# Kernel tuning notes

Hardware: AMD Instinct MI355X
Metric: run time of the kernel (lower is better)

The kernel has to match this reference:

```python
import jax, jax.numpy as jnp
import numpy as np

N_NODES = 100000
N_PART = 5000
N_EDGES = 1000000
D_NODE = 128
D_PART = 128
D_ATT = 20


def setup_inputs() -> dict:
    key = jax.random.key(0)
    ks = jax.random.split(key, 20)
    inp = {
        "nodes_hidden": jax.random.normal(ks[0], (N_NODES, D_NODE), jnp.float32),
        "particles_hidden": jax.random.normal(ks[1], (N_PART, D_PART), jnp.float32),
        "global_rep": jax.random.normal(ks[2], (N_PART, D_NODE), jnp.float32),
        "src": jax.random.randint(ks[3], (N_EDGES,), 0, N_NODES, jnp.int32),
        "dst": jax.random.randint(ks[4], (N_EDGES,), 0, N_PART, jnp.int32),
        "key_W": jax.random.normal(ks[5], (D_NODE, D_ATT), jnp.float32) * 0.05,
        "key_b": jnp.zeros((D_ATT,), jnp.float32),
        "val_W": jax.random.normal(ks[6], (D_NODE, D_PART), jnp.float32) * 0.05,
        "val_b": jnp.zeros((D_PART,), jnp.float32),
        "q_W": jax.random.normal(ks[7], (D_PART + D_NODE, D_ATT), jnp.float32) * 0.05,
        "q_b": jnp.zeros((D_ATT,), jnp.float32),
        "W_ih": jax.random.normal(ks[8], (3 * D_PART, D_PART), jnp.float32) * 0.05,
        "W_hh": jax.random.normal(ks[9], (3 * D_PART, D_PART), jnp.float32) * 0.05,
        "b_ih": jnp.zeros((3 * D_PART,), jnp.float32),
        "b_hh": jnp.zeros((3 * D_PART,), jnp.float32),
        "ln_g": jnp.ones((D_PART,), jnp.float32),
        "ln_b": jnp.zeros((D_PART,), jnp.float32),
        "mlp_W1": jax.random.normal(ks[10], (D_PART, 64), jnp.float32) * 0.05,
        "mlp_b1": jnp.zeros((64,), jnp.float32),
        "mlp_W2": jax.random.normal(ks[11], (64, D_PART), jnp.float32) * 0.05,
        "mlp_b2": jnp.zeros((D_PART,), jnp.float32),
    }
    return inp


def reference(nodes_hidden, particles_hidden, global_rep, src, dst,
              key_W, key_b, val_W, val_b, q_W, q_b,
              W_ih, W_hh, b_ih, b_hh, ln_g, ln_b,
              mlp_W1, mlp_b1, mlp_W2, mlp_b2):
    norm = jnp.float32(1.0) / jnp.sqrt(jnp.float32(D_ATT))
    keys = nodes_hidden @ key_W + key_b          # [N, 20]
    vals = nodes_hidden @ val_W + val_b          # [N, P]
    q_in = jnp.concatenate([particles_hidden, global_rep], axis=1)
    query = q_in @ q_W + q_b                     # [Np, 20]

    # per-edge raw attention (ReLU'd copy in edges.data is unused downstream)
    att = jnp.sum(keys[src] * query[dst], axis=1) * norm     # [E]
    msg = att[:, None] * vals[src]                            # [E, P]
    weighted_sum = jax.ops.segment_sum(msg, dst, num_segments=particles_hidden.shape[0])

    # GRUCell(input=weighted_sum, hidden=particles_hidden), torch semantics
    gi = weighted_sum @ W_ih.T + b_ih
    gh = particles_hidden @ W_hh.T + b_hh
    i_r, i_z, i_n = jnp.split(gi, 3, axis=1)
    h_r, h_z, h_n = jnp.split(gh, 3, axis=1)
    r = jax.nn.sigmoid(i_r + h_r)
    z = jax.nn.sigmoid(i_z + h_z)
    n = jnp.tanh(i_n + r * h_n)
    h_new = (1.0 - z) * n + z * particles_hidden

    # LayerNorm (eps=1e-5)
    mu = jnp.mean(h_new, axis=-1, keepdims=True)
    var = jnp.mean(jnp.square(h_new - mu), axis=-1, keepdims=True)
    ln = (h_new - mu) * jax.lax.rsqrt(var + 1e-5) * ln_g + ln_b

    mlp_out = jax.nn.relu(ln @ mlp_W1 + mlp_b1) @ mlp_W2 + mlp_b2
    return particles_hidden + mlp_out
```

## Files before the change

### kernel.cpp

```cpp
#include <hip/hip_runtime.h>
#include <math.h>

#define N_NODES 100000
#define N_PART  5000
#define N_EDGES 1000000
#define D_NODE  128
#define D_PART  128
#define D_ATT   20
#define NBLK    128
#define EPB     ((N_EDGES + NBLK - 1) / NBLK)
#define TPV6    8
#define QBLKS   (N_PART / TPV6)

__device__ __forceinline__ float sigmoid_(float x) { return 1.f / (1.f + __expf(-x)); }
__device__ __forceinline__ float tanh_(float x)    { return 1.f - 2.f / (__expf(2.f * x) + 1.f); }

__device__ __forceinline__ void gru_body(float4 acc[4],
    float4 w0, float4 w1, float4 w2, float4 w3,
    float4 x0, float4 x1, float4 x2, float4 x3)
{
    acc[0].x += x0.x * w0.x + x0.y * w1.x + x0.z * w2.x + x0.w * w3.x;
    acc[0].y += x0.x * w0.y + x0.y * w1.y + x0.z * w2.y + x0.w * w3.y;
    acc[0].z += x0.x * w0.z + x0.y * w1.z + x0.z * w2.z + x0.w * w3.z;
    acc[0].w += x0.x * w0.w + x0.y * w1.w + x0.z * w2.w + x0.w * w3.w;
    acc[1].x += x1.x * w0.x + x1.y * w1.x + x1.z * w2.x + x1.w * w3.x;
    acc[1].y += x1.x * w0.y + x1.y * w1.y + x1.z * w2.y + x1.w * w3.y;
    acc[1].z += x1.x * w0.z + x1.y * w1.z + x1.z * w2.z + x1.w * w3.z;
    acc[1].w += x1.x * w0.w + x1.y * w1.w + x1.z * w2.w + x1.w * w3.w;
    acc[2].x += x2.x * w0.x + x2.y * w1.x + x2.z * w2.x + x2.w * w3.x;
    acc[2].y += x2.x * w0.y + x2.y * w1.y + x2.z * w2.y + x2.w * w3.y;
    acc[2].z += x2.x * w0.z + x2.y * w1.z + x2.z * w2.z + x2.w * w3.z;
    acc[2].w += x2.x * w0.w + x2.y * w1.w + x2.z * w2.w + x2.w * w3.w;
    acc[3].x += x3.x * w0.x + x3.y * w1.x + x3.z * w2.x + x3.w * w3.x;
    acc[3].y += x3.x * w0.y + x3.y * w1.y + x3.z * w2.y + x3.w * w3.y;
    acc[3].z += x3.x * w0.z + x3.y * w1.z + x3.z * w2.z + x3.w * w3.z;
    acc[3].w += x3.x * w0.w + x3.y * w1.w + x3.z * w2.w + x3.w * w3.w;
}

__global__ __launch_bounds__(256) void fused_front_kernel(
    const float* __restrict__ valW, const float* __restrict__ Wih,
    const float* __restrict__ Whh, float* __restrict__ Wbig,
    const float* __restrict__ valb, float* __restrict__ bvec,
    const int* __restrict__ dst, int* __restrict__ blockhist,
    const float* __restrict__ ph, const float* __restrict__ gr,
    const float* __restrict__ qW, const float* __restrict__ qb,
    const float* __restrict__ keyW, const float* __restrict__ keyb,
    float* __restrict__ qk, float* __restrict__ qoff)
{
    __shared__ float pool[5000];
    int blk = blockIdx.x;
    int t = threadIdx.x;

    if (blk < 12) {
        float (*sA)[33] = (float (*)[33])pool;
        float (*sB)[33] = (float (*)[33])(pool + 2112);
        int bk = blk / 6, bj = blk - bk * 6;
        int k0 = bk * 64, j0 = bj * 64;
        int tk = t >> 4, tj = t & 15;
        float acc[4][4];
        #pragma unroll
        for (int i = 0; i < 4; i++)
            #pragma unroll
            for (int j = 0; j < 4; j++) acc[i][j] = 0.f;

        for (int mc = 0; mc < 128; mc += 32) {
            #pragma unroll
            for (int s = 0; s < 2; s++) {
                int f = t + s * 256;
                int r = f >> 3, c4 = (f & 7) * 4;
                *(float4*)&sA[r][c4] = *(const float4*)(valW + (size_t)(k0 + r) * 128 + mc + c4);
                *(float4*)&sB[r][c4] = *(const float4*)(Wih  + (size_t)(j0 + r) * 128 + mc + c4);
            }
            __syncthreads();
            #pragma unroll 8
            for (int mm = 0; mm < 32; mm++) {
                float a0 = sA[tk * 4 + 0][mm], a1 = sA[tk * 4 + 1][mm];
                float a2 = sA[tk * 4 + 2][mm], a3 = sA[tk * 4 + 3][mm];
                float b0 = sB[tj * 4 + 0][mm], b1 = sB[tj * 4 + 1][mm];
                float b2 = sB[tj * 4 + 2][mm], b3 = sB[tj * 4 + 3][mm];
                acc[0][0] += a0 * b0; acc[0][1] += a0 * b1; acc[0][2] += a0 * b2; acc[0][3] += a0 * b3;
                acc[1][0] += a1 * b0; acc[1][1] += a1 * b1; acc[1][2] += a1 * b2; acc[1][3] += a1 * b3;
                acc[2][0] += a2 * b0; acc[2][1] += a2 * b1; acc[2][2] += a2 * b2; acc[2][3] += a2 * b3;
                acc[3][0] += a3 * b0; acc[3][1] += a3 * b1; acc[3][2] += a3 * b2; acc[3][3] += a3 * b3;
            }
            __syncthreads();
        }
        #pragma unroll
        for (int i = 0; i < 4; i++) {
            int k = k0 + tk * 4 + i;
            #pragma unroll
            for (int j = 0; j < 4; j++) {
                int oj = j0 + tj * 4 + j;
                Wbig[(size_t)k * 512 + (oj & 127) * 4 + (oj >> 7)] = acc[i][j];
            }
        }
    } else if (blk < 14) {
        for (int f = t; f < 8192; f += 256) {
            int e = (blk - 12) * 8192 + f;
            int k = e >> 7, c = e & 127;
            Wbig[(size_t)k * 512 + c * 4 + 3] = 0.f;
        }
    } else if (blk < 142) {
        #pragma unroll
        for (int s = 0; s < 2; s++) {
            int idx = 65536 + (blk - 14) * 512 + s * 256 + t;
            int k = idx >> 9;
            int jn = idx & 511;
            int j = (jn & 3) * 128 + (jn >> 2);
            int kp = k - 128;
            float v = 0.f;
            if (j < 256)       v = Whh[j * 128 + kp];
            else if (j >= 384) v = Whh[(j - 128) * 128 + kp];
            Wbig[(size_t)k * 512 + jn] = v;
        }
    } else if (blk < 144) {
        int c = (blk - 142) * 256 + t;
        if (c < 384) {
            float acc = 0.f;
            #pragma unroll 8
            for (int m = 0; m < 128; m++) acc += valb[m] * Wih[c * 128 + m];
            bvec[c] = acc;
        }
    } else if (blk < 272) {
        int b = blk - 144;
        int* h = (int*)pool;
        for (int i = t; i < N_PART; i += 256) h[i] = 0;
        __syncthreads();
        int beg = b * EPB, end = min(beg + EPB, N_EDGES);
        for (int e = beg + t; e < end; e += 256)
            atomicAdd(&h[dst[e]], 1);
        __syncthreads();
        for (int i = t; i < N_PART; i += 256)
            blockhist[(size_t)b * N_PART + i] = h[i];
    } else {
        float (*s_in)[260] = (float (*)[260])pool;
        float (*s_q)[20]   = (float (*)[20])(pool + 2080);
        float (*s_kw)[21]  = (float (*)[21])(pool + 2240);
        float* s_kb = pool + 4928;
        float* s_qb = pool + 4948;

        int pbase = (blk - 272) * TPV6;

        for (int f = t; f < TPV6 * 64; f += 256) {
            int pl = f >> 6, r = f & 63;
            int c4 = r * 4;
            int p = pbase + pl;
            float4 v;
            if (c4 < 128) v = *(const float4*)(ph + (size_t)p * 128 + c4);
            else          v = *(const float4*)(gr + (size_t)p * 128 + (c4 - 128));
            *(float4*)&s_in[pl][c4] = v;
        }
        for (int f = t; f < 2560; f += 256) {
            int j = f / 20, a = f - j * 20;
            s_kw[j][a] = keyW[f];
        }
        if (t < 20) { s_kb[t] = keyb[t]; s_qb[t] = qb[t]; }
        __syncthreads();

        if (t < 160) {
            int pl = t / 20, a = t - (t / 20) * 20;
            float acc = s_qb[a];
            const float* qwp = qW + a;
            #pragma unroll 8
            for (int k = 0; k < 256; k++) acc += s_in[pl][k] * qwp[k * 20];
            s_q[pl][a] = acc;
        }
        __syncthreads();

        {
            int pl = t >> 5, j0 = (t & 31) * 4;
            float acc0 = 0.f, acc1 = 0.f, acc2 = 0.f, acc3 = 0.f;
            #pragma unroll
            for (int a = 0; a < 20; a++) {
                float qv = s_q[pl][a];
                acc0 += qv * s_kw[j0][a];
                acc1 += qv * s_kw[j0 + 1][a];
                acc2 += qv * s_kw[j0 + 2][a];
                acc3 += qv * s_kw[j0 + 3][a];
            }
            float4 o; o.x = acc0; o.y = acc1; o.z = acc2; o.w = acc3;
            *(float4*)(qk + (size_t)(pbase + pl) * 128 + j0) = o;

            if (t < TPV6) {
                float acc = 0.f;
                #pragma unroll
                for (int a = 0; a < 20; a++) acc += s_kb[a] * s_q[t][a];
                qoff[pbase + t] = acc;
            }
        }
    }
}

__global__ __launch_bounds__(256) void colscan_kernel(
    int* __restrict__ blockhist, int* __restrict__ totals)
{
    int i = blockIdx.x * 256 + threadIdx.x;
    if (i >= N_PART) return;
    int run = 0;
    for (int b = 0; b < NBLK; b++) {
        size_t idx = (size_t)b * N_PART + i;
        int v = blockhist[idx];
        blockhist[idx] = run;
        run += v;
    }
    totals[i] = run;
}

__global__ __launch_bounds__(256) void scan_kernel(
    const int* __restrict__ totals, int* __restrict__ offsets)
{
    __shared__ int ss[256];
    int t = threadIdx.x;
    const int CH = 20;
    int beg = t * CH;
    int end = min(beg + CH, N_PART);
    int lsum = 0;
    for (int i = beg; i < end; i++) lsum += totals[i];
    ss[t] = lsum;
    __syncthreads();
    for (int off = 1; off < 256; off <<= 1) {
        int v = (t >= off) ? ss[t - off] : 0;
        __syncthreads();
        ss[t] += v;
        __syncthreads();
    }
    int base = ss[t] - lsum;
    for (int i = beg; i < end; i++) {
        offsets[i] = base;
        base += totals[i];
    }
    if (t == 0) offsets[N_PART] = N_EDGES;
}

__global__ __launch_bounds__(256) void scatter_sorted_kernel(
    const int* __restrict__ src, const int* __restrict__ dst,
    const int* __restrict__ offsets, const int* __restrict__ blockhist,
    int* __restrict__ ssrc)
{
    __shared__ int cur[N_PART];
    int b = blockIdx.x;
    for (int i = threadIdx.x; i < N_PART; i += 256)
        cur[i] = offsets[i] + blockhist[(size_t)b * N_PART + i];
    __syncthreads();
    int beg = b * EPB, end = min(beg + EPB, N_EDGES);
    for (int e = beg + threadIdx.x; e < end; e += 256) {
        int d = dst[e];
        int pos = atomicAdd(&cur[d], 1);
        ssrc[pos] = src[e];
    }
}

__global__ __launch_bounds__(256) void edge_agg_kernel(
    const float* __restrict__ nodes, const float* __restrict__ qk,
    const float* __restrict__ qoff,
    const int* __restrict__ offsets, const int* __restrict__ ssrc,
    float* __restrict__ agg, float* __restrict__ att_sum)
{
    const float norm = 0.22360679774997896f;
    int p = blockIdx.x;
    int tid = threadIdx.x;
    int lane = tid & 63;
    int wave = tid >> 6;
    int half = lane >> 5;
    int colq = (lane & 31) * 4;

    const float4 q = *(const float4*)(qk + (size_t)p * 128 + colq);
    float qo = qoff[p];
    int beg = offsets[p], end = offsets[p + 1];
    int n = end - beg;
    int np = (n + 1) >> 1;
    int npfull = n >> 1;

    float4 a = {0.f, 0.f, 0.f, 0.f};
    float asum = 0.f;

    int pi = wave;
    for (; pi + 12 < npfull; pi += 16) {
        int e0 = beg + 2 * pi + half;
        int s0 = ssrc[e0];
        int s1 = ssrc[e0 + 8];
        int s2 = ssrc[e0 + 16];
        int s3 = ssrc[e0 + 24];
        float4 x0 = *(const float4*)(nodes + (size_t)s0 * 128 + colq);
        float4 x1 = *(const float4*)(nodes + (size_t)s1 * 128 + colq);
        float4 x2 = *(const float4*)(nodes + (size_t)s2 * 128 + colq);
        float4 x3 = *(const float4*)(nodes + (size_t)s3 * 128 + colq);
        float d0 = x0.x * q.x + x0.y * q.y + x0.z * q.z + x0.w * q.w;
        float d1 = x1.x * q.x + x1.y * q.y + x1.z * q.z + x1.w * q.w;
        float d2 = x2.x * q.x + x2.y * q.y + x2.z * q.z + x2.w * q.w;
        float d3 = x3.x * q.x + x3.y * q.y + x3.z * q.z + x3.w * q.w;
        #pragma unroll
        for (int off = 1; off <= 16; off <<= 1) {
            d0 += __shfl_xor(d0, off, 64);
            d1 += __shfl_xor(d1, off, 64);
            d2 += __shfl_xor(d2, off, 64);
            d3 += __shfl_xor(d3, off, 64);
        }
        float t0 = (d0 + qo) * norm;
        float t1 = (d1 + qo) * norm;
        float t2 = (d2 + qo) * norm;
        float t3 = (d3 + qo) * norm;
        a.x += t0 * x0.x + t1 * x1.x + t2 * x2.x + t3 * x3.x;
        a.y += t0 * x0.y + t1 * x1.y + t2 * x2.y + t3 * x3.y;
        a.z += t0 * x0.z + t1 * x1.z + t2 * x2.z + t3 * x3.z;
        a.w += t0 * x0.w + t1 * x1.w + t2 * x2.w + t3 * x3.w;
        asum += t0 + t1 + t2 + t3;
    }
    for (; pi < np; pi += 4) {
        int e0 = beg + 2 * pi;
        bool has1 = (e0 + 1 < end);
        int s0 = ssrc[e0];
        int s1 = has1 ? ssrc[e0 + 1] : s0;
        int s = half ? s1 : s0;
        float4 x = *(const float4*)(nodes + (size_t)s * 128 + colq);
        float d = x.x * q.x + x.y * q.y + x.z * q.z + x.w * q.w;
        #pragma unroll
        for (int off = 1; off <= 16; off <<= 1) d += __shfl_xor(d, off, 64);
        float att = (d + qo) * norm;
        if (half && !has1) att = 0.f;
        a.x += att * x.x; a.y += att * x.y; a.z += att * x.z; a.w += att * x.w;
        asum += att;
    }

    a.x += __shfl_xor(a.x, 32, 64);
    a.y += __shfl_xor(a.y, 32, 64);
    a.z += __shfl_xor(a.z, 32, 64);
    a.w += __shfl_xor(a.w, 32, 64);
    asum += __shfl_xor(asum, 32, 64);

    __shared__ float s_acc[4][128];
    __shared__ float s_as[4];
    if (lane < 32) {
        *(float4*)&s_acc[wave][colq] = a;
        if (lane == 0) s_as[wave] = asum;
    }
    __syncthreads();

    if (tid < 128) {
        float v = s_acc[0][tid] + s_acc[1][tid] + s_acc[2][tid] + s_acc[3][tid];
        agg[(size_t)p * 128 + tid] = v;
        if (tid == 0) att_sum[p] = s_as[0] + s_as[1] + s_as[2] + s_as[3];
    }
}

__global__ __launch_bounds__(256) void gru_fused_v6(
    const float* __restrict__ agg, const float* __restrict__ att_sum,
    const float* __restrict__ ph,
    const float* __restrict__ Wbig, const float* __restrict__ bvec,
    const float* __restrict__ bih, const float* __restrict__ bhh,
    const float* __restrict__ lng, const float* __restrict__ lnb,
    const float* __restrict__ W1, const float* __restrict__ b1,
    const float* __restrict__ W2, const float* __restrict__ b2,
    float* __restrict__ out)
{
    __shared__ float s_in[TPV6][256];
    __shared__ float s_ln[TPV6][128];
    __shared__ float s_hid[TPV6][64];

    int t = threadIdx.x;
    int pbase = blockIdx.x * TPV6;

    for (int f = t; f < TPV6 * 64; f += 256) {
        int pl = f >> 6, r = f & 63;
        int c4 = r * 4;
        int p = pbase + pl;
        float4 v;
        if (c4 < 128) v = *(const float4*)(agg + (size_t)p * 128 + c4);
        else          v = *(const float4*)(ph + (size_t)p * 128 + (c4 - 128));
        *(float4*)&s_in[pl][c4] = v;
    }

    int c  = t & 127;
    int j4 = c * 4;
    int pg = t >> 7;
    float4 cb, bv;
    cb.x = bih[c]       + bhh[c];        bv.x = bvec[c];
    cb.y = bih[128 + c] + bhh[128 + c];  bv.y = bvec[128 + c];
    cb.z = bih[256 + c];                 bv.z = bvec[256 + c];
    cb.w = bhh[256 + c];                 bv.w = 0.f;
    float4 acc[4];
    #pragma unroll
    for (int i = 0; i < 4; i++) {
        float as = att_sum[pbase + pg * 4 + i];
        acc[i].x = cb.x + as * bv.x;
        acc[i].y = cb.y + as * bv.y;
        acc[i].z = cb.z + as * bv.z;
        acc[i].w = cb.w + as * bv.w;
    }
    __syncthreads();

    const float* wp = Wbig + j4;
    float4 w0 = *(const float4*)(wp);
    float4 w1 = *(const float4*)(wp + 512);
    float4 w2 = *(const float4*)(wp + 1024);
    float4 w3 = *(const float4*)(wp + 1536);
    float4 x0 = *(const float4*)&s_in[pg * 4 + 0][0];
    float4 x1 = *(const float4*)&s_in[pg * 4 + 1][0];
    float4 x2 = *(const float4*)&s_in[pg * 4 + 2][0];
    float4 x3 = *(const float4*)&s_in[pg * 4 + 3][0];
    for (int k = 0; k < 256; k += 4) {
        float4 cw0 = w0, cw1 = w1, cw2 = w2, cw3 = w3;
        float4 cx0 = x0, cx1 = x1, cx2 = x2, cx3 = x3;
        if (k < 252) {
            const float* wn = wp + (size_t)(k + 4) * 512;
            w0 = *(const float4*)(wn);
            w1 = *(const float4*)(wn + 512);
            w2 = *(const float4*)(wn + 1024);
            w3 = *(const float4*)(wn + 1536);
            x0 = *(const float4*)&s_in[pg * 4 + 0][k + 4];
            x1 = *(const float4*)&s_in[pg * 4 + 1][k + 4];
            x2 = *(const float4*)&s_in[pg * 4 + 2][k + 4];
            x3 = *(const float4*)&s_in[pg * 4 + 3][k + 4];
        }
        gru_body(acc, cw0, cw1, cw2, cw3, cx0, cx1, cx2, cx3);
    }

    #pragma unroll
    for (int i = 0; i < 4; i++) {
        int pl = pg * 4 + i;
        float r = sigmoid_(acc[i].x);
        float z = sigmoid_(acc[i].y);
        float n = tanh_(acc[i].z + r * acc[i].w);
        float h = s_in[pl][128 + c];
        s_ln[pl][c] = (1.f - z) * n + z * h;
    }
    __syncthreads();

    {
        int wv = t >> 6, l = t & 63;
        for (int pl = wv; pl < TPV6; pl += 4) {
            float v0 = s_ln[pl][l * 2], v1 = s_ln[pl][l * 2 + 1];
            float sum = v0 + v1, sq = v0 * v0 + v1 * v1;
            #pragma unroll
            for (int off = 1; off <= 32; off <<= 1) {
                sum += __shfl_xor(sum, off, 64);
                sq  += __shfl_xor(sq, off, 64);
            }
            float mu = sum * (1.f / 128.f);
            float var = sq * (1.f / 128.f) - mu * mu;
            float rstd = rsqrtf(var + 1e-5f);
            s_ln[pl][l * 2]     = (v0 - mu) * rstd * lng[l * 2] + lnb[l * 2];
            s_ln[pl][l * 2 + 1] = (v1 - mu) * rstd * lng[l * 2 + 1] + lnb[l * 2 + 1];
        }
    }
    __syncthreads();

    for (int idx = t; idx < TPV6 * 64; idx += 256) {
        int pl = idx >> 6, u = idx & 63;
        float a0 = b1[u];
        #pragma unroll 4
        for (int k = 0; k < 128; k++) a0 += s_ln[pl][k] * W1[k * 64 + u];
        s_hid[pl][u] = fmaxf(a0, 0.f);
    }
    __syncthreads();

    for (int idx = t; idx < TPV6 * 32; idx += 256) {
        int pl = idx >> 5, qd = idx & 31;
        int c4 = qd * 4;
        float4 o = *(const float4*)(b2 + c4);
        #pragma unroll 4
        for (int u = 0; u < 64; u++) {
            float av = s_hid[pl][u];
            float4 w = *(const float4*)(W2 + u * 128 + c4);
            o.x += av * w.x; o.y += av * w.y; o.z += av * w.z; o.w += av * w.w;
        }
        float4 h4 = *(const float4*)&s_in[pl][128 + c4];
        float4 res;
        res.x = h4.x + o.x; res.y = h4.y + o.y;
        res.z = h4.z + o.z; res.w = h4.w + o.w;
        *(float4*)(out + (size_t)(pbase + pl) * 128 + c4) = res;
    }
}

extern "C" void kernel_launch(void* const* d_in, const int* in_sizes, int n_in,
                              void* d_out, int out_size, void* d_ws, size_t ws_size,
                              hipStream_t stream) {
    const float* nodes = (const float*)d_in[0];
    const float* ph    = (const float*)d_in[1];
    const float* gr    = (const float*)d_in[2];
    const int*   src   = (const int*)d_in[3];
    const int*   dst   = (const int*)d_in[4];
    const float* keyW  = (const float*)d_in[5];
    const float* keyb  = (const float*)d_in[6];
    const float* valW  = (const float*)d_in[7];
    const float* valb  = (const float*)d_in[8];
    const float* qW    = (const float*)d_in[9];
    const float* qb    = (const float*)d_in[10];
    const float* Wih   = (const float*)d_in[11];
    const float* Whh   = (const float*)d_in[12];
    const float* bih   = (const float*)d_in[13];
    const float* bhh   = (const float*)d_in[14];
    const float* lng   = (const float*)d_in[15];
    const float* lnb   = (const float*)d_in[16];
    const float* W1    = (const float*)d_in[17];
    const float* b1    = (const float*)d_in[18];
    const float* W2    = (const float*)d_in[19];
    const float* b2    = (const float*)d_in[20];
    float* out = (float*)d_out;

    float* ws_f      = (float*)d_ws;
    float* qk        = ws_f;
    float* qoff      = qk + 640000;
    float* agg       = qoff + 5008;
    float* att_sum   = agg + 640000;
    int*   totals    = (int*)(att_sum + 5008);
    int*   offsets   = totals + 5008;
    int*   blockhist = offsets + 5008;
    int*   ssrc      = blockhist + (size_t)NBLK * N_PART;
    float* Wbig      = (float*)(ssrc + 1000000);
    float* bvec      = Wbig + 131072;

    fused_front_kernel<<<272 + QBLKS, 256, 0, stream>>>(
        valW, Wih, Whh, Wbig,
        valb, bvec,
        dst, blockhist,
        ph, gr, qW, qb, keyW, keyb, qk, qoff);

    colscan_kernel<<<(N_PART + 255) / 256, 256, 0, stream>>>(blockhist, totals);

    scan_kernel<<<1, 256, 0, stream>>>(totals, offsets);

    scatter_sorted_kernel<<<NBLK, 256, 0, stream>>>(src, dst, offsets, blockhist, ssrc);

    edge_agg_kernel<<<N_PART, 256, 0, stream>>>(nodes, qk, qoff, offsets, ssrc, agg, att_sum);

    gru_fused_v6<<<N_PART / TPV6, 256, 0, stream>>>(
        agg, att_sum, ph, Wbig, bvec, bih, bhh, lng, lnb, W1, b1, W2, b2, out);
}
```

Baseline: 283.5 us.

## Gather node features as bf16 in edge aggregation to halve gather bytes

Adds 1024 extra blocks to the front kernel that convert nodes_hidden to bf16 with round-to-nearest-even, then runs a new edge aggregation kernel that gathers 8-byte bf16 rows instead of 16-byte fp32 rows. The aim is to cut the random-gather memory traffic of the 1M-edge aggregation, which dominates runtime. In exchange it adds a full 51MB read and 25MB write conversion pass, and it lowers the precision of the keys/values contribution. The new path is used only when the workspace is large enough.

```diff
diff --git a/kernel.cpp b/kernel.cpp
--- a/kernel.cpp
+++ b/kernel.cpp
@@ -11,9 +11,19 @@
 #define EPB     ((N_EDGES + NBLK - 1) / NBLK)
 #define TPV6    8
 #define QBLKS   (N_PART / TPV6)
+#define CVTBLKS 1024
 
 __device__ __forceinline__ float sigmoid_(float x) { return 1.f / (1.f + __expf(-x)); }
 __device__ __forceinline__ float tanh_(float x)    { return 1.f - 2.f / (__expf(2.f * x) + 1.f); }
+
+__device__ __forceinline__ float4 bf4_to_f4(uint2 r) {
+    float4 f;
+    f.x = __uint_as_float(r.x << 16);
+    f.y = __uint_as_float(r.x & 0xFFFF0000u);
+    f.z = __uint_as_float(r.y << 16);
+    f.w = __uint_as_float(r.y & 0xFFFF0000u);
+    return f;
+}
 
 __device__ __forceinline__ void gru_body(float4 acc[4],
     float4 w0, float4 w1, float4 w2, float4 w3,
@@ -45,7 +55,8 @@
     const float* __restrict__ ph, const float* __restrict__ gr,
     const float* __restrict__ qW, const float* __restrict__ qb,
     const float* __restrict__ keyW, const float* __restrict__ keyb,
-    float* __restrict__ qk, float* __restrict__ qoff)
+    float* __restrict__ qk, float* __restrict__ qoff,
+    const float* __restrict__ nodes, unsigned short* __restrict__ nodes_bf)
 {
     __shared__ float pool[5000];
     int blk = blockIdx.x;
@@ -132,7 +143,7 @@
         __syncthreads();
         for (int i = t; i < N_PART; i += 256)
             blockhist[(size_t)b * N_PART + i] = h[i];
-    } else {
+    } else if (blk < 897) {
         float (*s_in)[260] = (float (*)[260])pool;
         float (*s_q)[20]   = (float (*)[20])(pool + 2080);
         float (*s_kw)[21]  = (float (*)[21])(pool + 2240);
@@ -188,6 +199,29 @@
                 qoff[pbase + t] = acc;
             }
         }
+    } else {
+        const uint64_t total8 = (uint64_t)N_NODES * 128 / 8;
+        uint64_t cb = (uint64_t)(blk - 897) * 256 + t;
+        const uint32_t* inb = (const uint32_t*)nodes;
+        uint32_t* outb = (uint32_t*)nodes_bf;
+        for (uint64_t c = cb; c < total8; c += (uint64_t)CVTBLKS * 256) {
+            uint4 a = *(const uint4*)(inb + c * 8);
+            uint4 b = *(const uint4*)(inb + c * 8 + 4);
+            uint32_t r0 = (a.x + 0x7FFFu + ((a.x >> 16) & 1u)) >> 16;
+            uint32_t r1 = (a.y + 0x7FFFu + ((a.y >> 16) & 1u)) >> 16;
+            uint32_t r2 = (a.z + 0x7FFFu + ((a.z >> 16) & 1u)) >> 16;
+            uint32_t r3 = (a.w + 0x7FFFu + ((a.w >> 16) & 1u)) >> 16;
+            uint32_t r4 = (b.x + 0x7FFFu + ((b.x >> 16) & 1u)) >> 16;
+            uint32_t r5 = (b.y + 0x7FFFu + ((b.y >> 16) & 1u)) >> 16;
+            uint32_t r6 = (b.z + 0x7FFFu + ((b.z >> 16) & 1u)) >> 16;
+            uint32_t r7 = (b.w + 0x7FFFu + ((b.w >> 16) & 1u)) >> 16;
+            uint4 o;
+            o.x = r0 | (r1 << 16);
+            o.y = r2 | (r3 << 16);
+            o.z = r4 | (r5 << 16);
+            o.w = r6 | (r7 << 16);
+            *(uint4*)(outb + c * 4) = o;
+        }
     }
 }
 
@@ -247,6 +281,104 @@
         int d = dst[e];
         int pos = atomicAdd(&cur[d], 1);
         ssrc[pos] = src[e];
+    }
+}
+
+__global__ __launch_bounds__(256) void edge_agg_bf16_kernel(
+    const unsigned short* __restrict__ nodes_bf, const float* __restrict__ qk,
+    const float* __restrict__ qoff,
+    const int* __restrict__ offsets, const int* __restrict__ ssrc,
+    float* __restrict__ agg, float* __restrict__ att_sum)
+{
+    const float norm = 0.22360679774997896f;
+    int p = blockIdx.x;
+    int tid = threadIdx.x;
+    int lane = tid & 63;
+    int wave = tid >> 6;
+    int half = lane >> 5;
+    int colq = (lane & 31) * 4;
+
+    const float4 q = *(const float4*)(qk + (size_t)p * 128 + colq);
+    float qo = qoff[p];
+    int beg = offsets[p], end = offsets[p + 1];
+    int n = end - beg;
+    int np = (n + 1) >> 1;
+    int npfull = n >> 1;
+
+    float4 a = {0.f, 0.f, 0.f, 0.f};
+    float asum = 0.f;
+
+    int pi = wave;
+    for (; pi + 12 < npfull; pi += 16) {
+        int e0 = beg + 2 * pi + half;
+        int s0 = ssrc[e0];
+        int s1 = ssrc[e0 + 8];
+        int s2 = ssrc[e0 + 16];
+        int s3 = ssrc[e0 + 24];
+        uint2 r0 = *(const uint2*)(nodes_bf + (size_t)s0 * 128 + colq);
+        uint2 r1 = *(const uint2*)(nodes_bf + (size_t)s1 * 128 + colq);
+        uint2 r2 = *(const uint2*)(nodes_bf + (size_t)s2 * 128 + colq);
+        uint2 r3 = *(const uint2*)(nodes_bf + (size_t)s3 * 128 + colq);
+        float4 x0 = bf4_to_f4(r0);
+        float4 x1 = bf4_to_f4(r1);
+        float4 x2 = bf4_to_f4(r2);
+        float4 x3 = bf4_to_f4(r3);
+        float d0 = x0.x * q.x + x0.y * q.y + x0.z * q.z + x0.w * q.w;
+        float d1 = x1.x * q.x + x1.y * q.y + x1.z * q.z + x1.w * q.w;
+        float d2 = x2.x * q.x + x2.y * q.y + x2.z * q.z + x2.w * q.w;
+        float d3 = x3.x * q.x + x3.y * q.y + x3.z * q.z + x3.w * q.w;
+        #pragma unroll
+        for (int off = 1; off <= 16; off <<= 1) {
+            d0 += __shfl_xor(d0, off, 64);
+            d1 += __shfl_xor(d1, off, 64);
+            d2 += __shfl_xor(d2, off, 64);
+            d3 += __shfl_xor(d3, off, 64);
+        }
+        float t0 = (d0 + qo) * norm;
+        float t1 = (d1 + qo) * norm;
+        float t2 = (d2 + qo) * norm;
+        float t3 = (d3 + qo) * norm;
+        a.x += t0 * x0.x + t1 * x1.x + t2 * x2.x + t3 * x3.x;
+        a.y += t0 * x0.y + t1 * x1.y + t2 * x2.y + t3 * x3.y;
+        a.z += t0 * x0.z + t1 * x1.z + t2 * x2.z + t3 * x3.z;
+        a.w += t0 * x0.w + t1 * x1.w + t2 * x2.w + t3 * x3.w;
+        asum += t0 + t1 + t2 + t3;
+    }
+    for (; pi < np; pi += 4) {
+        int e0 = beg + 2 * pi;
+        bool has1 = (e0 + 1 < end);
+        int s0 = ssrc[e0];
+        int s1 = has1 ? ssrc[e0 + 1] : s0;
+        int s = half ? s1 : s0;
+        uint2 r = *(const uint2*)(nodes_bf + (size_t)s * 128 + colq);
+        float4 x = bf4_to_f4(r);
+        float d = x.x * q.x + x.y * q.y + x.z * q.z + x.w * q.w;
+        #pragma unroll
+        for (int off = 1; off <= 16; off <<= 1) d += __shfl_xor(d, off, 64);
+        float att = (d + qo) * norm;
+        if (half && !has1) att = 0.f;
+        a.x += att * x.x; a.y += att * x.y; a.z += att * x.z; a.w += att * x.w;
+        asum += att;
+    }
+
+    a.x += __shfl_xor(a.x, 32, 64);
+    a.y += __shfl_xor(a.y, 32, 64);
+    a.z += __shfl_xor(a.z, 32, 64);
+    a.w += __shfl_xor(a.w, 32, 64);
+    asum += __shfl_xor(asum, 32, 64);
+
+    __shared__ float s_acc[4][128];
+    __shared__ float s_as[4];
+    if (lane < 32) {
+        *(float4*)&s_acc[wave][colq] = a;
+        if (lane == 0) s_as[wave] = asum;
+    }
+    __syncthreads();
+
+    if (tid < 128) {
+        float v = s_acc[0][tid] + s_acc[1][tid] + s_acc[2][tid] + s_acc[3][tid];
+        agg[(size_t)p * 128 + tid] = v;
+        if (tid == 0) att_sum[p] = s_as[0] + s_as[1] + s_as[2] + s_as[3];
     }
 }
 
@@ -509,12 +641,16 @@
     int*   ssrc      = blockhist + (size_t)NBLK * N_PART;
     float* Wbig      = (float*)(ssrc + 1000000);
     float* bvec      = Wbig + 131072;
-
-    fused_front_kernel<<<272 + QBLKS, 256, 0, stream>>>(
+    unsigned short* nodes_bf = (unsigned short*)(bvec + 512);
+
+    int do_bf = (ws_size >= (size_t)38000000) ? 1 : 0;
+
+    fused_front_kernel<<<897 + (do_bf ? CVTBLKS : 0), 256, 0, stream>>>(
         valW, Wih, Whh, Wbig,
         valb, bvec,
         dst, blockhist,
-        ph, gr, qW, qb, keyW, keyb, qk, qoff);
+        ph, gr, qW, qb, keyW, keyb, qk, qoff,
+        nodes, nodes_bf);
 
     colscan_kernel<<<(N_PART + 255) / 256, 256, 0, stream>>>(blockhist, totals);
 
@@ -522,7 +658,10 @@
 
     scatter_sorted_kernel<<<NBLK, 256, 0, stream>>>(src, dst, offsets, blockhist, ssrc);
 
-    edge_agg_kernel<<<N_PART, 256, 0, stream>>>(nodes, qk, qoff, offsets, ssrc, agg, att_sum);
+    if (do_bf)
+        edge_agg_bf16_kernel<<<N_PART, 256, 0, stream>>>(nodes_bf, qk, qoff, offsets, ssrc, agg, att_sum);
+    else
+        edge_agg_kernel<<<N_PART, 256, 0, stream>>>(nodes, qk, qoff, offsets, ssrc, agg, att_sum);
 
     gru_fused_v6<<<N_PART / TPV6, 256, 0, stream>>>(
         agg, att_sum, ph, Wbig, bvec, bih, bhh, lng, lnb, W1, b1, W2, b2, out);
```

Measured after the change: 275.8 us. 2.7% less time.

## Gather node features and GRU weights in bf16 to halve memory traffic

Applied to the files above, without the earlier changes.

Adds a conversion stage inside the front kernel that rounds node features to bf16. The edge aggregation kernel then gathers half-width rows and widens them in registers. GRU weights are also stored as a packed bf16 layout and expanded on load. The aim is to cut gather and weight bandwidth, at the cost of an extra full pass over the node table and reduced precision.

```diff
diff --git a/kernel.cpp b/kernel.cpp
--- a/kernel.cpp
+++ b/kernel.cpp
@@ -11,9 +11,24 @@
 #define EPB     ((N_EDGES + NBLK - 1) / NBLK)
 #define TPV6    8
 #define QBLKS   (N_PART / TPV6)
+#define CVTBLKS 1024
 
 __device__ __forceinline__ float sigmoid_(float x) { return 1.f / (1.f + __expf(-x)); }
 __device__ __forceinline__ float tanh_(float x)    { return 1.f - 2.f / (__expf(2.f * x) + 1.f); }
+
+__device__ __forceinline__ float4 bf4_to_f4(uint2 r) {
+    float4 f;
+    f.x = __uint_as_float(r.x << 16);
+    f.y = __uint_as_float(r.x & 0xFFFF0000u);
+    f.z = __uint_as_float(r.y << 16);
+    f.w = __uint_as_float(r.y & 0xFFFF0000u);
+    return f;
+}
+
+__device__ __forceinline__ unsigned short f_to_bf(float v) {
+    uint32_t u = __float_as_uint(v);
+    return (unsigned short)((u + 0x7FFFu + ((u >> 16) & 1u)) >> 16);
+}
 
 __device__ __forceinline__ void gru_body(float4 acc[4],
     float4 w0, float4 w1, float4 w2, float4 w3,
@@ -37,15 +52,20 @@
     acc[3].w += x3.x * w0.w + x3.y * w1.w + x3.z * w2.w + x3.w * w3.w;
 }
 
+__device__ __forceinline__ size_t wpk_idx(int k, int jn) {
+    return ((size_t)(k >> 1) * 128 + (jn >> 2)) * 8 + ((k & 1) << 2) + (jn & 3);
+}
+
 __global__ __launch_bounds__(256) void fused_front_kernel(
     const float* __restrict__ valW, const float* __restrict__ Wih,
-    const float* __restrict__ Whh, float* __restrict__ Wbig,
+    const float* __restrict__ Whh, unsigned short* __restrict__ Wpack,
     const float* __restrict__ valb, float* __restrict__ bvec,
     const int* __restrict__ dst, int* __restrict__ blockhist,
     const float* __restrict__ ph, const float* __restrict__ gr,
     const float* __restrict__ qW, const float* __restrict__ qb,
     const float* __restrict__ keyW, const float* __restrict__ keyb,
-    float* __restrict__ qk, float* __restrict__ qoff)
+    float* __restrict__ qk, float* __restrict__ qoff,
+    const float* __restrict__ nodes, unsigned short* __restrict__ nodes_bf)
 {
     __shared__ float pool[5000];
     int blk = blockIdx.x;
@@ -91,14 +111,15 @@
             #pragma unroll
             for (int j = 0; j < 4; j++) {
                 int oj = j0 + tj * 4 + j;
-                Wbig[(size_t)k * 512 + (oj & 127) * 4 + (oj >> 7)] = acc[i][j];
+                int jn = (oj & 127) * 4 + (oj >> 7);
+                Wpack[wpk_idx(k, jn)] = f_to_bf(acc[i][j]);
             }
         }
     } else if (blk < 14) {
         for (int f = t; f < 8192; f += 256) {
             int e = (blk - 12) * 8192 + f;
             int k = e >> 7, c = e & 127;
-            Wbig[(size_t)k * 512 + c * 4 + 3] = 0.f;
+            Wpack[wpk_idx(k, c * 4 + 3)] = 0;
         }
     } else if (blk < 142) {
         #pragma unroll
@@ -111,7 +132,7 @@
             float v = 0.f;
             if (j < 256)       v = Whh[j * 128 + kp];
             else if (j >= 384) v = Whh[(j - 128) * 128 + kp];
-            Wbig[(size_t)k * 512 + jn] = v;
+            Wpack[wpk_idx(k, jn)] = f_to_bf(v);
         }
     } else if (blk < 144) {
         int c = (blk - 142) * 256 + t;
@@ -132,7 +153,7 @@
         __syncthreads();
         for (int i = t; i < N_PART; i += 256)
             blockhist[(size_t)b * N_PART + i] = h[i];
-    } else {
+    } else if (blk < 897) {
         float (*s_in)[260] = (float (*)[260])pool;
         float (*s_q)[20]   = (float (*)[20])(pool + 2080);
         float (*s_kw)[21]  = (float (*)[21])(pool + 2240);
@@ -188,6 +209,29 @@
                 qoff[pbase + t] = acc;
             }
         }
+    } else {
+        const uint64_t total8 = (uint64_t)N_NODES * 128 / 8;
+        uint64_t cb = (uint64_t)(blk - 897) * 256 + t;
+        const uint32_t* inb = (const uint32_t*)nodes;
+        uint32_t* outb = (uint32_t*)nodes_bf;
+        for (uint64_t c = cb; c < total8; c += (uint64_t)CVTBLKS * 256) {
+            uint4 a = *(const uint4*)(inb + c * 8);
+            uint4 b = *(const uint4*)(inb + c * 8 + 4);
+            uint32_t r0 = (a.x + 0x7FFFu + ((a.x >> 16) & 1u)) >> 16;
+            uint32_t r1 = (a.y + 0x7FFFu + ((a.y >> 16) & 1u)) >> 16;
+            uint32_t r2 = (a.z + 0x7FFFu + ((a.z >> 16) & 1u)) >> 16;
+            uint32_t r3 = (a.w + 0x7FFFu + ((a.w >> 16) & 1u)) >> 16;
+            uint32_t r4 = (b.x + 0x7FFFu + ((b.x >> 16) & 1u)) >> 16;
+            uint32_t r5 = (b.y + 0x7FFFu + ((b.y >> 16) & 1u)) >> 16;
+            uint32_t r6 = (b.z + 0x7FFFu + ((b.z >> 16) & 1u)) >> 16;
+            uint32_t r7 = (b.w + 0x7FFFu + ((b.w >> 16) & 1u)) >> 16;
+            uint4 o;
+            o.x = r0 | (r1 << 16);
+            o.y = r2 | (r3 << 16);
+            o.z = r4 | (r5 << 16);
+            o.w = r6 | (r7 << 16);
+            *(uint4*)(outb + c * 4) = o;
+        }
     }
 }
 
@@ -250,8 +294,8 @@
     }
 }
 
-__global__ __launch_bounds__(256) void edge_agg_kernel(
-    const float* __restrict__ nodes, const float* __restrict__ qk,
+__global__ __launch_bounds__(256) void edge_agg_bf16_kernel(
+    const unsigned short* __restrict__ nodes_bf, const float* __restrict__ qk,
     const float* __restrict__ qoff,
     const int* __restrict__ offsets, const int* __restrict__ ssrc,
     float* __restrict__ agg, float* __restrict__ att_sum)
@@ -281,10 +325,14 @@
         int s1 = ssrc[e0 + 8];
         int s2 = ssrc[e0 + 16];
         int s3 = ssrc[e0 + 24];
-        float4 x0 = *(const float4*)(nodes + (size_t)s0 * 128 + colq);
-        float4 x1 = *(const float4*)(nodes + (size_t)s1 * 128 + colq);
-        float4 x2 = *(const float4*)(nodes + (size_t)s2 * 128 + colq);
-        float4 x3 = *(const float4*)(nodes + (size_t)s3 * 128 + colq);
+        uint2 r0 = *(const uint2*)(nodes_bf + (size_t)s0 * 128 + colq);
+        uint2 r1 = *(const uint2*)(nodes_bf + (size_t)s1 * 128 + colq);
+        uint2 r2 = *(const uint2*)(nodes_bf + (size_t)s2 * 128 + colq);
+        uint2 r3 = *(const uint2*)(nodes_bf + (size_t)s3 * 128 + colq);
+        float4 x0 = bf4_to_f4(r0);
+        float4 x1 = bf4_to_f4(r1);
+        float4 x2 = bf4_to_f4(r2);
+        float4 x3 = bf4_to_f4(r3);
         float d0 = x0.x * q.x + x0.y * q.y + x0.z * q.z + x0.w * q.w;
         float d1 = x1.x * q.x + x1.y * q.y + x1.z * q.z + x1.w * q.w;
         float d2 = x2.x * q.x + x2.y * q.y + x2.z * q.z + x2.w * q.w;
@@ -312,7 +360,8 @@
         int s0 = ssrc[e0];
         int s1 = has1 ? ssrc[e0 + 1] : s0;
         int s = half ? s1 : s0;
-        float4 x = *(const float4*)(nodes + (size_t)s * 128 + colq);
+        uint2 r = *(const uint2*)(nodes_bf + (size_t)s * 128 + colq);
+        float4 x = bf4_to_f4(r);
         float d = x.x * q.x + x.y * q.y + x.z * q.z + x.w * q.w;
         #pragma unroll
         for (int off = 1; off <= 16; off <<= 1) d += __shfl_xor(d, off, 64);
@@ -343,10 +392,10 @@
     }
 }
 
-__global__ __launch_bounds__(256) void gru_fused_v6(
+__global__ __launch_bounds__(256) void gru_fused_v8(
     const float* __restrict__ agg, const float* __restrict__ att_sum,
     const float* __restrict__ ph,
-    const float* __restrict__ Wbig, const float* __restrict__ bvec,
+    const unsigned short* __restrict__ Wpack, const float* __restrict__ bvec,
     const float* __restrict__ bih, const float* __restrict__ bhh,
     const float* __restrict__ lng, const float* __restrict__ lnb,
     const float* __restrict__ W1, const float* __restrict__ b1,
@@ -371,7 +420,6 @@
     }
 
     int c  = t & 127;
-    int j4 = c * 4;
     int pg = t >> 7;
     float4 cb, bv;
     cb.x = bih[c]       + bhh[c];        bv.x = bvec[c];
@@ -389,30 +437,30 @@
     }
     __syncthreads();
 
-    const float* wp = Wbig + j4;
-    float4 w0 = *(const float4*)(wp);
-    float4 w1 = *(const float4*)(wp + 512);
-    float4 w2 = *(const float4*)(wp + 1024);
-    float4 w3 = *(const float4*)(wp + 1536);
+    const uint4* wpk = (const uint4*)Wpack;
+    uint4 wu = wpk[c];
+    uint4 wv = wpk[128 + c];
     float4 x0 = *(const float4*)&s_in[pg * 4 + 0][0];
     float4 x1 = *(const float4*)&s_in[pg * 4 + 1][0];
     float4 x2 = *(const float4*)&s_in[pg * 4 + 2][0];
     float4 x3 = *(const float4*)&s_in[pg * 4 + 3][0];
     for (int k = 0; k < 256; k += 4) {
-        float4 cw0 = w0, cw1 = w1, cw2 = w2, cw3 = w3;
+        uint4 cu = wu, cv = wv;
         float4 cx0 = x0, cx1 = x1, cx2 = x2, cx3 = x3;
         if (k < 252) {
-            const float* wn = wp + (size_t)(k + 4) * 512;
-            w0 = *(const float4*)(wn);
-            w1 = *(const float4*)(wn + 512);
-            w2 = *(const float4*)(wn + 1024);
-            w3 = *(const float4*)(wn + 1536);
+            int k2n = (k >> 1) + 2;
+            wu = wpk[(size_t)k2n * 128 + c];
+            wv = wpk[(size_t)(k2n + 1) * 128 + c];
             x0 = *(const float4*)&s_in[pg * 4 + 0][k + 4];
             x1 = *(const float4*)&s_in[pg * 4 + 1][k + 4];
             x2 = *(const float4*)&s_in[pg * 4 + 2][k + 4];
             x3 = *(const float4*)&s_in[pg * 4 + 3][k + 4];
         }
-        gru_body(acc, cw0, cw1, cw2, cw3, cx0, cx1, cx2, cx3);
+        float4 w0 = bf4_to_f4(make_uint2(cu.x, cu.y));
+        float4 w1 = bf4_to_f4(make_uint2(cu.z, cu.w));
+        float4 w2 = bf4_to_f4(make_uint2(cv.x, cv.y));
+        float4 w3 = bf4_to_f4(make_uint2(cv.z, cv.w));
+        gru_body(acc, w0, w1, w2, w3, cx0, cx1, cx2, cx3);
     }
 
     #pragma unroll
@@ -427,8 +475,8 @@
     __syncthreads();
 
     {
-        int wv = t >> 6, l = t & 63;
-        for (int pl = wv; pl < TPV6; pl += 4) {
+        int wv2 = t >> 6, l = t & 63;
+        for (int pl = wv2; pl < TPV6; pl += 4) {
             float v0 = s_ln[pl][l * 2], v1 = s_ln[pl][l * 2 + 1];
             float sum = v0 + v1, sq = v0 * v0 + v1 * v1;
             #pragma unroll
@@ -507,14 +555,16 @@
     int*   offsets   = totals + 5008;
     int*   blockhist = offsets + 5008;
     int*   ssrc      = blockhist + (size_t)NBLK * N_PART;
-    float* Wbig      = (float*)(ssrc + 1000000);
-    float* bvec      = Wbig + 131072;
-
-    fused_front_kernel<<<272 + QBLKS, 256, 0, stream>>>(
-        valW, Wih, Whh, Wbig,
+    unsigned short* Wpack = (unsigned short*)(ssrc + 1000000);
+    float* bvec      = (float*)(Wpack + 131072);
+    unsigned short* nodes_bf = (unsigned short*)(bvec + 512);
+
+    fused_front_kernel<<<897 + CVTBLKS, 256, 0, stream>>>(
+        valW, Wih, Whh, Wpack,
         valb, bvec,
         dst, blockhist,
-        ph, gr, qW, qb, keyW, keyb, qk, qoff);
+        ph, gr, qW, qb, keyW, keyb, qk, qoff,
+        nodes, nodes_bf);
 
     colscan_kernel<<<(N_PART + 255) / 256, 256, 0, stream>>>(blockhist, totals);
 
@@ -522,8 +572,8 @@
 
     scatter_sorted_kernel<<<NBLK, 256, 0, stream>>>(src, dst, offsets, blockhist, ssrc);
 
-    edge_agg_kernel<<<N_PART, 256, 0, stream>>>(nodes, qk, qoff, offsets, ssrc, agg, att_sum);
-
-    gru_fused_v6<<<N_PART / TPV6, 256, 0, stream>>>(
-        agg, att_sum, ph, Wbig, bvec, bih, bhh, lng, lnb, W1, b1, W2, b2, out);
-}
+    edge_agg_bf16_kernel<<<N_PART, 256, 0, stream>>>(nodes_bf, qk, qoff, offsets, ssrc, agg, att_sum);
+
+    gru_fused_v8<<<N_PART / TPV6, 256, 0, stream>>>(
+        agg, att_sum, ph, Wpack, bvec, bih, bhh, lng, lnb, W1, b1, W2, b2, out);
+}
```

Result: faster. 269.3 us (-5.0%).
